# Kernel tuning notes

Hardware: AMD Instinct MI355X
Metric: run time of the kernel (lower is better)

Reference implementation:

```python
import jax, jax.numpy as jnp
import numpy as np

T, B, I, H, C, O = 4096, 8, 256, 512, 1024, 512
SCHEDULE = 1.0
UPPER_T = 0.3
NIND = int((1.0 - SCHEDULE) * (C - 2) * UPPER_T) + 1  # = 1 (argmax WTA)


def setup_inputs() -> dict:
    key = jax.random.key(0)
    ks = jax.random.split(key, 8)
    def lin(k, fan_out, fan_in):
        s = 1.0 / np.sqrt(fan_in)
        kw, kb = jax.random.split(k)
        return (jax.random.uniform(kw, (fan_out, fan_in), jnp.float32, -s, s),
                jax.random.uniform(kb, (fan_out,), jnp.float32, -s, s))
    i2m_w, i2m_b = lin(ks[0], H, I)
    m2h_w, m2h_b = lin(ks[1], C, H)
    h2o_w, h2o_b = lin(ks[2], O, C)
    return {
        "x": jax.random.normal(ks[3], (T, B, I), jnp.float32),
        "hidden1": jnp.zeros((1,), jnp.float32),  # unused dummy (overwritten in torch forward)
        "i2m_w": i2m_w, "i2m_b": i2m_b,
        "m2h_w": m2h_w, "m2h_b": m2h_b,
        "h2o_w": h2o_w, "h2o_b": h2o_b,
    }


def reference(x, hidden1, i2m_w, i2m_b, m2h_w, m2h_b, h2o_w, h2o_b):
    # linear -> relu
    h = jax.nn.relu(jnp.einsum('tbi,hi->tbh', x, i2m_w) + i2m_b)
    # linear -> relu -> concept pre-activations [T,B,C]
    c = jax.nn.relu(jnp.einsum('tbh,ch->tbc', h, m2h_w) + m2h_b)
    # winner-take-all: top-Nind scatter mask (replaces CPU argsort round-trip)
    _, idx = jax.lax.top_k(c, NIND)  # [T,B,NIND]
    t_ix = jnp.arange(c.shape[0])[:, None, None]
    b_ix = jnp.arange(c.shape[1])[None, :, None]
    mask = jnp.zeros_like(c).at[t_ix, b_ix, idx].set(1.0)
    m = c * mask
    # L2 normalize over concept axis
    m = m / jnp.linalg.norm(m, axis=-1, keepdims=True)
    out = jnp.einsum('tbc,oc->tbo', m, h2o_w) + h2o_b
    return jax.nn.log_softmax(out, axis=-1)
```

## Files before the change

kernel.cpp:

```cpp
#include <hip/hip_runtime.h>
#include <stdint.h>

#define M_ROWS 32768
#define I_DIM 256
#define H_DIM 512
#define C_DIM 1024
#define O_DIM 512

typedef __attribute__((ext_vector_type(8))) short bf16x8;
typedef __attribute__((ext_vector_type(4))) float f32x4;

__device__ __forceinline__ ushort bf16_rne(float f) {
    unsigned u = __float_as_uint(f);
    unsigned r = u + 0x7FFFu + ((u >> 16) & 1u);
    return (ushort)(r >> 16);
}
__device__ __forceinline__ float bf16_f32(ushort h) {
    return __uint_as_float(((unsigned)h) << 16);
}
__device__ __forceinline__ void split2(float f, ushort& hi, ushort& mid) {
    hi = bf16_rne(f);
    mid = bf16_rne(f - bf16_f32(hi));
}

__device__ __forceinline__ void async_ld16(const void* g, void* l) {
    __builtin_amdgcn_global_load_lds(
        (const __attribute__((address_space(1))) void*)g,
        (__attribute__((address_space(3))) void*)l, 16, 0, 0);
}

__device__ __forceinline__ unsigned long long packvi(float v, int col) {
    unsigned u = __float_as_uint(v);
    u = (u & 0x80000000u) ? ~u : (u | 0x80000000u);
    return ((unsigned long long)u << 32) | (unsigned)(~col);
}

__global__ __launch_bounds__(256)
void wsplit(const float* __restrict__ W, ushort* __restrict__ hi,
            ushort* __restrict__ mid) {
    int i = (blockIdx.x * 256 + threadIdx.x) * 4;
    float4 v = *(const float4*)(W + i);
    ushort4 hv, mv;
    split2(v.x, hv.x, mv.x);
    split2(v.y, hv.y, mv.y);
    split2(v.z, hv.z, mv.z);
    split2(v.w, hv.w, mv.w);
    *(ushort4*)(hi + i) = hv;
    *(ushort4*)(mid + i) = mv;
}

__global__ __launch_bounds__(256, 3)
void gemm1_mfma(const float* __restrict__ X, const ushort* __restrict__ W1h,
                const ushort* __restrict__ W1m, const float* __restrict__ b1,
                unsigned int* __restrict__ Hp) {
    __shared__ __align__(16) ushort As[2][128 * 32];
    __shared__ __align__(16) ushort Bs[2][128 * 32];
    const int tid = threadIdx.x;
    const int lane = tid & 63, wave = tid >> 6;
    const int wm = wave >> 1, wn = wave & 1;
    const int lcol = lane & 15, quad = lane >> 4;
    const int mBase = blockIdx.x * 128;
    const int nBase = blockIdx.y * 128;
    const int s_row = tid >> 1, s_half = tid & 1;
    const int bplane = wave >> 1;
    const ushort* wp = bplane ? W1m : W1h;
    const int brow0 = (wave & 1) * 64;

    f32x4 acc[4][4];
    #pragma unroll
    for (int i = 0; i < 4; ++i)
        #pragma unroll
        for (int j = 0; j < 4; ++j)
            acc[i][j] = (f32x4){0.f, 0.f, 0.f, 0.f};

    int aoff[4], boff[4];
    #pragma unroll
    for (int t = 0; t < 4; ++t) {
        aoff[t] = (wm * 64 + t * 16 + lcol) * 32 + quad * 8;
        boff[t] = (wn * 64 + t * 16 + lcol) * 32 + quad * 8;
    }

    for (int ks = 0; ks < I_DIM / 32; ++ks) {
        const int k0 = ks * 32;
        const float* ap = X + (size_t)(mBase + s_row) * I_DIM + k0 + s_half * 16;
        float4 f0 = ((const float4*)ap)[0];
        float4 f1 = ((const float4*)ap)[1];
        float4 f2 = ((const float4*)ap)[2];
        float4 f3 = ((const float4*)ap)[3];

        __syncthreads();

        #pragma unroll
        for (int i = 0; i < 4; ++i) {
            int r = brow0 + i * 16;
            const ushort* g = wp + (size_t)(nBase + r + (lane >> 2)) * I_DIM
                              + k0 + (lane & 3) * 8;
            async_ld16(g, &Bs[bplane][r * 32]);
        }

        float f[16];
        *(float4*)&f[0] = f0; *(float4*)&f[4] = f1;
        *(float4*)&f[8] = f2; *(float4*)&f[12] = f3;
        bf16x8 h0, h1, m0, m1;
        #pragma unroll
        for (int j = 0; j < 8; ++j) {
            ushort hu, mu;
            split2(f[j], hu, mu);
            h0[j] = (short)hu; m0[j] = (short)mu;
            split2(f[j + 8], hu, mu);
            h1[j] = (short)hu; m1[j] = (short)mu;
        }
        int dst = s_row * 32 + s_half * 16;
        int sw = (s_row >> 1) & 1;
        *(bf16x8*)&As[0][dst + sw * 8]     = sw ? h1 : h0;
        *(bf16x8*)&As[0][dst + 8 - sw * 8] = sw ? h0 : h1;
        *(bf16x8*)&As[1][dst + sw * 8]     = sw ? m1 : m0;
        *(bf16x8*)&As[1][dst + 8 - sw * 8] = sw ? m0 : m1;

        __syncthreads();

        bf16x8 af[4][2];
        #pragma unroll
        for (int mt = 0; mt < 4; ++mt) {
            af[mt][0] = *(const bf16x8*)&As[0][aoff[mt]];
            af[mt][1] = *(const bf16x8*)&As[1][aoff[mt]];
        }
        #pragma unroll
        for (int nt = 0; nt < 4; ++nt) {
            bf16x8 bh = *(const bf16x8*)&Bs[0][boff[nt]];
            bf16x8 bm = *(const bf16x8*)&Bs[1][boff[nt]];
            #pragma unroll
            for (int mt = 0; mt < 4; ++mt) {
                f32x4 a = acc[mt][nt];
                a = __builtin_amdgcn_mfma_f32_16x16x32_bf16(af[mt][1], bm, a, 0, 0, 0);
                a = __builtin_amdgcn_mfma_f32_16x16x32_bf16(af[mt][1], bh, a, 0, 0, 0);
                a = __builtin_amdgcn_mfma_f32_16x16x32_bf16(af[mt][0], bm, a, 0, 0, 0);
                a = __builtin_amdgcn_mfma_f32_16x16x32_bf16(af[mt][0], bh, a, 0, 0, 0);
                acc[mt][nt] = a;
            }
        }
    }

    #pragma unroll
    for (int nt = 0; nt < 4; ++nt) {
        int col = nBase + wn * 64 + nt * 16 + lcol;
        float bias = b1[col];
        #pragma unroll
        for (int mt = 0; mt < 4; ++mt) {
            #pragma unroll
            for (int r = 0; r < 4; ++r) {
                int row = mBase + wm * 64 + mt * 16 + quad * 4 + r;
                float v = fmaxf(acc[mt][nt][r] + bias, 0.f);
                ushort hu, mu;
                split2(v, hu, mu);
                Hp[(size_t)row * H_DIM + col] = ((unsigned)hu << 16) | (unsigned)mu;
            }
        }
    }
}

__global__ __launch_bounds__(256, 3)
void gemm2_mfma(const unsigned int* __restrict__ Hp,
                const ushort* __restrict__ W2h, const ushort* __restrict__ W2m,
                const float* __restrict__ b2,
                unsigned long long* __restrict__ part) {
    __shared__ __align__(16) ushort As[2][128 * 32];
    __shared__ __align__(16) ushort Bs[2][128 * 32];
    const int tid = threadIdx.x;
    const int lane = tid & 63, wave = tid >> 6;
    const int wm = wave >> 1, wn = wave & 1;
    const int lcol = lane & 15, quad = lane >> 4;
    const int mBase = blockIdx.x * 128;
    const int nBase = blockIdx.y * 128;
    const int s_row = tid >> 1, s_half = tid & 1;
    const int bplane = wave >> 1;
    const ushort* wp = bplane ? W2m : W2h;
    const int brow0 = (wave & 1) * 64;

    f32x4 acc[4][4];
    #pragma unroll
    for (int i = 0; i < 4; ++i)
        #pragma unroll
        for (int j = 0; j < 4; ++j)
            acc[i][j] = (f32x4){0.f, 0.f, 0.f, 0.f};

    int aoff[4], boff[4];
    #pragma unroll
    for (int t = 0; t < 4; ++t) {
        aoff[t] = (wm * 64 + t * 16 + lcol) * 32 + quad * 8;
        boff[t] = (wn * 64 + t * 16 + lcol) * 32 + quad * 8;
    }

    for (int ks = 0; ks < H_DIM / 32; ++ks) {
        const int k0 = ks * 32;
        const unsigned int* ap = Hp + (size_t)(mBase + s_row) * H_DIM + k0 + s_half * 16;
        uint4 a0 = ((const uint4*)ap)[0];
        uint4 a1 = ((const uint4*)ap)[1];
        uint4 a2 = ((const uint4*)ap)[2];
        uint4 a3 = ((const uint4*)ap)[3];

        __syncthreads();

        #pragma unroll
        for (int i = 0; i < 4; ++i) {
            int r = brow0 + i * 16;
            const ushort* g = wp + (size_t)(nBase + r + (lane >> 2)) * H_DIM
                              + k0 + (lane & 3) * 8;
            async_ld16(g, &Bs[bplane][r * 32]);
        }

        unsigned int w[16];
        *(uint4*)&w[0] = a0;  *(uint4*)&w[4] = a1;
        *(uint4*)&w[8] = a2;  *(uint4*)&w[12] = a3;
        bf16x8 h0, h1, m0, m1;
        #pragma unroll
        for (int j = 0; j < 8; ++j) {
            h0[j] = (short)(w[j] >> 16);     m0[j] = (short)(w[j] & 0xFFFFu);
            h1[j] = (short)(w[j + 8] >> 16); m1[j] = (short)(w[j + 8] & 0xFFFFu);
        }
        int dst = s_row * 32 + s_half * 16;
        int sw = (s_row >> 1) & 1;
        *(bf16x8*)&As[0][dst + sw * 8]     = sw ? h1 : h0;
        *(bf16x8*)&As[0][dst + 8 - sw * 8] = sw ? h0 : h1;
        *(bf16x8*)&As[1][dst + sw * 8]     = sw ? m1 : m0;
        *(bf16x8*)&As[1][dst + 8 - sw * 8] = sw ? m0 : m1;

        __syncthreads();

        bf16x8 af[4][2];
        #pragma unroll
        for (int mt = 0; mt < 4; ++mt) {
            af[mt][0] = *(const bf16x8*)&As[0][aoff[mt]];
            af[mt][1] = *(const bf16x8*)&As[1][aoff[mt]];
        }
        #pragma unroll
        for (int nt = 0; nt < 4; ++nt) {
            bf16x8 bh = *(const bf16x8*)&Bs[0][boff[nt]];
            bf16x8 bm = *(const bf16x8*)&Bs[1][boff[nt]];
            #pragma unroll
            for (int mt = 0; mt < 4; ++mt) {
                f32x4 a = acc[mt][nt];
                a = __builtin_amdgcn_mfma_f32_16x16x32_bf16(af[mt][1], bm, a, 0, 0, 0);
                a = __builtin_amdgcn_mfma_f32_16x16x32_bf16(af[mt][1], bh, a, 0, 0, 0);
                a = __builtin_amdgcn_mfma_f32_16x16x32_bf16(af[mt][0], bm, a, 0, 0, 0);
                a = __builtin_amdgcn_mfma_f32_16x16x32_bf16(af[mt][0], bh, a, 0, 0, 0);
                acc[mt][nt] = a;
            }
        }
    }

    unsigned long long best[4][4];
    #pragma unroll
    for (int mt = 0; mt < 4; ++mt)
        #pragma unroll
        for (int r = 0; r < 4; ++r)
            best[mt][r] = 0ull;

    #pragma unroll
    for (int nt = 0; nt < 4; ++nt) {
        int col = nBase + wn * 64 + nt * 16 + lcol;
        float bias = b2[col];
        #pragma unroll
        for (int mt = 0; mt < 4; ++mt) {
            #pragma unroll
            for (int r = 0; r < 4; ++r) {
                float v = acc[mt][nt][r] + bias;
                unsigned long long p = packvi(v, col);
                if (p > best[mt][r]) best[mt][r] = p;
            }
        }
    }
    #pragma unroll
    for (int mt = 0; mt < 4; ++mt)
        #pragma unroll
        for (int r = 0; r < 4; ++r) {
            unsigned long long b = best[mt][r];
            #pragma unroll
            for (int off = 1; off < 16; off <<= 1) {
                unsigned long long o = __shfl_xor((long long)b, off, 64);
                if (o > b) b = o;
            }
            best[mt][r] = b;
        }

    __syncthreads();
    unsigned long long* red = (unsigned long long*)&As[0][0];
    if (lcol == 0) {
        #pragma unroll
        for (int mt = 0; mt < 4; ++mt)
            #pragma unroll
            for (int r = 0; r < 4; ++r)
                red[(wm * 64 + mt * 16 + quad * 4 + r) * 2 + wn] = best[mt][r];
    }
    __syncthreads();
    if (tid < 128) {
        unsigned long long a = red[tid * 2], b = red[tid * 2 + 1];
        part[(size_t)(mBase + tid) * 8 + blockIdx.y] = (a > b) ? a : b;
    }
}

__global__ __launch_bounds__(256)
void argmax_reduce(const unsigned long long* __restrict__ part, int* __restrict__ jstar) {
    int m = blockIdx.x * blockDim.x + threadIdx.x;
    if (m >= M_ROWS) return;
    const unsigned long long* p = part + (size_t)m * 8;
    unsigned long long best = p[0];
    #pragma unroll
    for (int t = 1; t < 8; ++t) {
        unsigned long long q = p[t];
        if (q > best) best = q;
    }
    unsigned u = (unsigned)(best >> 32);
    float v = (u & 0x80000000u) ? __uint_as_float(u ^ 0x80000000u)
                                : __uint_as_float(~u);
    int col = (int)(~(unsigned)best) & (C_DIM - 1);
    jstar[m] = (v > 0.f) ? col : 0;
}

__global__ __launch_bounds__(256)
void ls_table(const float* __restrict__ Wo, const float* __restrict__ bo,
              float* __restrict__ LS) {
    const int j = blockIdx.x;
    const int t = threadIdx.x;
    __shared__ float sred[4];

    float l0 = Wo[(size_t)t * C_DIM + j] + bo[t];
    float l1 = Wo[(size_t)(t + 256) * C_DIM + j] + bo[t + 256];

    float mx = fmaxf(l0, l1);
    #pragma unroll
    for (int off = 1; off < 64; off <<= 1)
        mx = fmaxf(mx, __shfl_xor(mx, off, 64));
    if ((t & 63) == 0) sred[t >> 6] = mx;
    __syncthreads();
    mx = fmaxf(fmaxf(sred[0], sred[1]), fmaxf(sred[2], sred[3]));
    __syncthreads();

    float s = expf(l0 - mx) + expf(l1 - mx);
    #pragma unroll
    for (int off = 1; off < 64; off <<= 1)
        s += __shfl_xor(s, off, 64);
    if ((t & 63) == 0) sred[t >> 6] = s;
    __syncthreads();
    s = sred[0] + sred[1] + sred[2] + sred[3];

    float lse = mx + logf(s);
    LS[(size_t)j * O_DIM + t] = l0 - lse;
    LS[(size_t)j * O_DIM + t + 256] = l1 - lse;
}

__global__ __launch_bounds__(256)
void gather_out(const int* __restrict__ jstar, const float* __restrict__ LS,
                float* __restrict__ out) {
    int idx = blockIdx.x * blockDim.x + threadIdx.x;
    int m = idx >> 7;
    int q = idx & 127;
    float4 v = ((const float4*)LS)[((size_t)jstar[m] << 7) + q];
    ((float4*)out)[idx] = v;
}

extern "C" void kernel_launch(void* const* d_in, const int* in_sizes, int n_in,
                              void* d_out, int out_size, void* d_ws, size_t ws_size,
                              hipStream_t stream) {
    const float* x     = (const float*)d_in[0];
    const float* i2m_w = (const float*)d_in[2];
    const float* i2m_b = (const float*)d_in[3];
    const float* m2h_w = (const float*)d_in[4];
    const float* m2h_b = (const float*)d_in[5];
    const float* h2o_w = (const float*)d_in[6];
    const float* h2o_b = (const float*)d_in[7];
    float* out = (float*)d_out;

    char* ws = (char*)d_ws;
    ushort* w1h = (ushort*)(ws);
    ushort* w1m = (ushort*)(ws + 262144);
    ushort* w2h = (ushort*)(ws + 524288);
    ushort* w2m = (ushort*)(ws + 1572864);
    unsigned long long* part = (unsigned long long*)(ws + 2621440);
    int*   jstar = (int*)(ws + 4718592);
    float* LS    = (float*)(ws);

    unsigned int* Hp = (unsigned int*)d_out;

    wsplit<<<(H_DIM * I_DIM) / 1024, 256, 0, stream>>>(i2m_w, w1h, w1m);
    wsplit<<<(C_DIM * H_DIM) / 1024, 256, 0, stream>>>(m2h_w, w2h, w2m);
    gemm1_mfma<<<dim3(M_ROWS / 128, H_DIM / 128), 256, 0, stream>>>(
        x, w1h, w1m, i2m_b, Hp);
    gemm2_mfma<<<dim3(M_ROWS / 128, C_DIM / 128), 256, 0, stream>>>(
        Hp, w2h, w2m, m2h_b, part);
    argmax_reduce<<<M_ROWS / 256, 256, 0, stream>>>(part, jstar);
    ls_table<<<C_DIM, 256, 0, stream>>>(h2o_w, h2o_b, LS);
    gather_out<<<(M_ROWS * (O_DIM / 4)) / 256, 256, 0, stream>>>(jstar, LS, out);
}
```

Before: 280.9 us.

## Fuse prep kernels, drop mid*mid MFMA, split H planes, atomicMax argmax

The two weight-split kernels, the log-softmax table and the zeroing of the argmax buffer are merged into one prep launch. gemm1 now writes separate hi and mid bf16 planes of H, so gemm2 can fill shared memory directly with async global-to-LDS loads instead of unpacking through registers. The mid*mid MFMA term is dropped in both GEMMs, and occupancy is raised to 4 blocks per SM. The per-row argmax now goes through atomicMax on a single 64-bit slot, which removes the separate reduce kernel. Dropping the mid*mid product lowers precision slightly, and the async LDS path loses the old bank-swizzle on the A tile.

```diff
diff --git a/kernel.cpp b/kernel.cpp
--- a/kernel.cpp
+++ b/kernel.cpp
@@ -36,23 +36,60 @@
 }
 
 __global__ __launch_bounds__(256)
-void wsplit(const float* __restrict__ W, ushort* __restrict__ hi,
-            ushort* __restrict__ mid) {
-    int i = (blockIdx.x * 256 + threadIdx.x) * 4;
-    float4 v = *(const float4*)(W + i);
-    ushort4 hv, mv;
-    split2(v.x, hv.x, mv.x);
-    split2(v.y, hv.y, mv.y);
-    split2(v.z, hv.z, mv.z);
-    split2(v.w, hv.w, mv.w);
-    *(ushort4*)(hi + i) = hv;
-    *(ushort4*)(mid + i) = mv;
-}
-
-__global__ __launch_bounds__(256, 3)
+void prep(const float* __restrict__ W1, ushort* __restrict__ w1h, ushort* __restrict__ w1m,
+          const float* __restrict__ W2, ushort* __restrict__ w2h, ushort* __restrict__ w2m,
+          const float* __restrict__ Wo, const float* __restrict__ bo,
+          float* __restrict__ LS, unsigned long long* __restrict__ part) {
+    __shared__ float sred[4];
+    const int b = blockIdx.x;
+    const int t = threadIdx.x;
+    if (b < 640) {
+        const float* W = (b < 128) ? W1 : W2;
+        ushort* hh = (b < 128) ? w1h : w2h;
+        ushort* mm = (b < 128) ? w1m : w2m;
+        int i = ((b < 128 ? b : b - 128) * 256 + t) * 4;
+        float4 v = *(const float4*)(W + i);
+        ushort4 hv, mv;
+        split2(v.x, hv.x, mv.x);
+        split2(v.y, hv.y, mv.y);
+        split2(v.z, hv.z, mv.z);
+        split2(v.w, hv.w, mv.w);
+        *(ushort4*)(hh + i) = hv;
+        *(ushort4*)(mm + i) = mv;
+    } else if (b < 1664) {
+        const int j = b - 640;
+        float l0 = Wo[(size_t)t * C_DIM + j] + bo[t];
+        float l1 = Wo[(size_t)(t + 256) * C_DIM + j] + bo[t + 256];
+
+        float mx = fmaxf(l0, l1);
+        #pragma unroll
+        for (int off = 1; off < 64; off <<= 1)
+            mx = fmaxf(mx, __shfl_xor(mx, off, 64));
+        if ((t & 63) == 0) sred[t >> 6] = mx;
+        __syncthreads();
+        mx = fmaxf(fmaxf(sred[0], sred[1]), fmaxf(sred[2], sred[3]));
+        __syncthreads();
+
+        float s = expf(l0 - mx) + expf(l1 - mx);
+        #pragma unroll
+        for (int off = 1; off < 64; off <<= 1)
+            s += __shfl_xor(s, off, 64);
+        if ((t & 63) == 0) sred[t >> 6] = s;
+        __syncthreads();
+        s = sred[0] + sred[1] + sred[2] + sred[3];
+
+        float lse = mx + logf(s);
+        LS[(size_t)j * O_DIM + t] = l0 - lse;
+        LS[(size_t)j * O_DIM + t + 256] = l1 - lse;
+    } else {
+        part[(b - 1664) * 256 + t] = 0ull;
+    }
+}
+
+__global__ __launch_bounds__(256, 4)
 void gemm1_mfma(const float* __restrict__ X, const ushort* __restrict__ W1h,
                 const ushort* __restrict__ W1m, const float* __restrict__ b1,
-                unsigned int* __restrict__ Hp) {
+                ushort* __restrict__ Hh, ushort* __restrict__ Hm) {
     __shared__ __align__(16) ushort As[2][128 * 32];
     __shared__ __align__(16) ushort Bs[2][128 * 32];
     const int tid = threadIdx.x;
@@ -65,6 +102,7 @@
     const int bplane = wave >> 1;
     const ushort* wp = bplane ? W1m : W1h;
     const int brow0 = (wave & 1) * 64;
+    const int lrow = lane >> 2, lk = (lane & 3) * 8;
 
     f32x4 acc[4][4];
     #pragma unroll
@@ -93,8 +131,7 @@
         #pragma unroll
         for (int i = 0; i < 4; ++i) {
             int r = brow0 + i * 16;
-            const ushort* g = wp + (size_t)(nBase + r + (lane >> 2)) * I_DIM
-                              + k0 + (lane & 3) * 8;
+            const ushort* g = wp + (size_t)(nBase + r + lrow) * I_DIM + k0 + lk;
             async_ld16(g, &Bs[bplane][r * 32]);
         }
 
@@ -132,7 +169,6 @@
             #pragma unroll
             for (int mt = 0; mt < 4; ++mt) {
                 f32x4 a = acc[mt][nt];
-                a = __builtin_amdgcn_mfma_f32_16x16x32_bf16(af[mt][1], bm, a, 0, 0, 0);
                 a = __builtin_amdgcn_mfma_f32_16x16x32_bf16(af[mt][1], bh, a, 0, 0, 0);
                 a = __builtin_amdgcn_mfma_f32_16x16x32_bf16(af[mt][0], bm, a, 0, 0, 0);
                 a = __builtin_amdgcn_mfma_f32_16x16x32_bf16(af[mt][0], bh, a, 0, 0, 0);
@@ -153,14 +189,15 @@
                 float v = fmaxf(acc[mt][nt][r] + bias, 0.f);
                 ushort hu, mu;
                 split2(v, hu, mu);
-                Hp[(size_t)row * H_DIM + col] = ((unsigned)hu << 16) | (unsigned)mu;
-            }
-        }
-    }
-}
-
-__global__ __launch_bounds__(256, 3)
-void gemm2_mfma(const unsigned int* __restrict__ Hp,
+                Hh[(size_t)row * H_DIM + col] = hu;
+                Hm[(size_t)row * H_DIM + col] = mu;
+            }
+        }
+    }
+}
+
+__global__ __launch_bounds__(256, 4)
+void gemm2_mfma(const ushort* __restrict__ Hh, const ushort* __restrict__ Hm,
                 const ushort* __restrict__ W2h, const ushort* __restrict__ W2m,
                 const float* __restrict__ b2,
                 unsigned long long* __restrict__ part) {
@@ -172,10 +209,16 @@
     const int lcol = lane & 15, quad = lane >> 4;
     const int mBase = blockIdx.x * 128;
     const int nBase = blockIdx.y * 128;
-    const int s_row = tid >> 1, s_half = tid & 1;
-    const int bplane = wave >> 1;
-    const ushort* wp = bplane ? W2m : W2h;
-    const int brow0 = (wave & 1) * 64;
+    const int lrow = lane >> 2, lk = (lane & 3) * 8;
+
+    const ushort* gsrc;
+    ushort* lbase;
+    switch (wave) {
+        case 0: gsrc = Hh  + (size_t)mBase * H_DIM; lbase = As[0]; break;
+        case 1: gsrc = Hm  + (size_t)mBase * H_DIM; lbase = As[1]; break;
+        case 2: gsrc = W2h + (size_t)nBase * H_DIM; lbase = Bs[0]; break;
+        default: gsrc = W2m + (size_t)nBase * H_DIM; lbase = Bs[1]; break;
+    }
 
     f32x4 acc[4][4];
     #pragma unroll
@@ -193,38 +236,12 @@
 
     for (int ks = 0; ks < H_DIM / 32; ++ks) {
         const int k0 = ks * 32;
-        const unsigned int* ap = Hp + (size_t)(mBase + s_row) * H_DIM + k0 + s_half * 16;
-        uint4 a0 = ((const uint4*)ap)[0];
-        uint4 a1 = ((const uint4*)ap)[1];
-        uint4 a2 = ((const uint4*)ap)[2];
-        uint4 a3 = ((const uint4*)ap)[3];
-
-        __syncthreads();
-
-        #pragma unroll
-        for (int i = 0; i < 4; ++i) {
-            int r = brow0 + i * 16;
-            const ushort* g = wp + (size_t)(nBase + r + (lane >> 2)) * H_DIM
-                              + k0 + (lane & 3) * 8;
-            async_ld16(g, &Bs[bplane][r * 32]);
-        }
-
-        unsigned int w[16];
-        *(uint4*)&w[0] = a0;  *(uint4*)&w[4] = a1;
-        *(uint4*)&w[8] = a2;  *(uint4*)&w[12] = a3;
-        bf16x8 h0, h1, m0, m1;
+        __syncthreads();
         #pragma unroll
         for (int j = 0; j < 8; ++j) {
-            h0[j] = (short)(w[j] >> 16);     m0[j] = (short)(w[j] & 0xFFFFu);
-            h1[j] = (short)(w[j + 8] >> 16); m1[j] = (short)(w[j + 8] & 0xFFFFu);
-        }
-        int dst = s_row * 32 + s_half * 16;
-        int sw = (s_row >> 1) & 1;
-        *(bf16x8*)&As[0][dst + sw * 8]     = sw ? h1 : h0;
-        *(bf16x8*)&As[0][dst + 8 - sw * 8] = sw ? h0 : h1;
-        *(bf16x8*)&As[1][dst + sw * 8]     = sw ? m1 : m0;
-        *(bf16x8*)&As[1][dst + 8 - sw * 8] = sw ? m0 : m1;
-
+            const ushort* g = gsrc + (size_t)(j * 16 + lrow) * H_DIM + k0 + lk;
+            async_ld16(g, lbase + j * 512);
+        }
         __syncthreads();
 
         bf16x8 af[4][2];
@@ -240,7 +257,6 @@
             #pragma unroll
             for (int mt = 0; mt < 4; ++mt) {
                 f32x4 a = acc[mt][nt];
-                a = __builtin_amdgcn_mfma_f32_16x16x32_bf16(af[mt][1], bm, a, 0, 0, 0);
                 a = __builtin_amdgcn_mfma_f32_16x16x32_bf16(af[mt][1], bh, a, 0, 0, 0);
                 a = __builtin_amdgcn_mfma_f32_16x16x32_bf16(af[mt][0], bm, a, 0, 0, 0);
                 a = __builtin_amdgcn_mfma_f32_16x16x32_bf16(af[mt][0], bh, a, 0, 0, 0);
@@ -249,114 +265,45 @@
         }
     }
 
-    unsigned long long best[4][4];
-    #pragma unroll
-    for (int mt = 0; mt < 4; ++mt)
-        #pragma unroll
-        for (int r = 0; r < 4; ++r)
-            best[mt][r] = 0ull;
-
-    #pragma unroll
-    for (int nt = 0; nt < 4; ++nt) {
-        int col = nBase + wn * 64 + nt * 16 + lcol;
-        float bias = b2[col];
-        #pragma unroll
-        for (int mt = 0; mt < 4; ++mt) {
-            #pragma unroll
-            for (int r = 0; r < 4; ++r) {
-                float v = acc[mt][nt][r] + bias;
+    #pragma unroll
+    for (int mt = 0; mt < 4; ++mt) {
+        #pragma unroll
+        for (int r = 0; r < 4; ++r) {
+            unsigned long long best = 0ull;
+            #pragma unroll
+            for (int nt = 0; nt < 4; ++nt) {
+                int col = nBase + wn * 64 + nt * 16 + lcol;
+                float v = acc[mt][nt][r] + b2[col];
                 unsigned long long p = packvi(v, col);
-                if (p > best[mt][r]) best[mt][r] = p;
-            }
-        }
-    }
-    #pragma unroll
-    for (int mt = 0; mt < 4; ++mt)
-        #pragma unroll
-        for (int r = 0; r < 4; ++r) {
-            unsigned long long b = best[mt][r];
+                if (p > best) best = p;
+            }
             #pragma unroll
             for (int off = 1; off < 16; off <<= 1) {
-                unsigned long long o = __shfl_xor((long long)b, off, 64);
-                if (o > b) b = o;
-            }
-            best[mt][r] = b;
-        }
-
-    __syncthreads();
-    unsigned long long* red = (unsigned long long*)&As[0][0];
-    if (lcol == 0) {
-        #pragma unroll
-        for (int mt = 0; mt < 4; ++mt)
-            #pragma unroll
-            for (int r = 0; r < 4; ++r)
-                red[(wm * 64 + mt * 16 + quad * 4 + r) * 2 + wn] = best[mt][r];
-    }
-    __syncthreads();
-    if (tid < 128) {
-        unsigned long long a = red[tid * 2], b = red[tid * 2 + 1];
-        part[(size_t)(mBase + tid) * 8 + blockIdx.y] = (a > b) ? a : b;
+                unsigned long long o = __shfl_xor((long long)best, off, 64);
+                if (o > best) best = o;
+            }
+            if (lcol == 0) {
+                int row = mBase + wm * 64 + mt * 16 + quad * 4 + r;
+                atomicMax(&part[row], best);
+            }
+        }
     }
 }
 
 __global__ __launch_bounds__(256)
-void argmax_reduce(const unsigned long long* __restrict__ part, int* __restrict__ jstar) {
-    int m = blockIdx.x * blockDim.x + threadIdx.x;
-    if (m >= M_ROWS) return;
-    const unsigned long long* p = part + (size_t)m * 8;
-    unsigned long long best = p[0];
-    #pragma unroll
-    for (int t = 1; t < 8; ++t) {
-        unsigned long long q = p[t];
-        if (q > best) best = q;
-    }
+void gather_out(const unsigned long long* __restrict__ part,
+                const float* __restrict__ LS, float* __restrict__ out) {
+    const int tid = threadIdx.x;
+    const int row = blockIdx.x * 2 + (tid >> 7);
+    const int q = tid & 127;
+    unsigned long long best = part[row];
     unsigned u = (unsigned)(best >> 32);
     float v = (u & 0x80000000u) ? __uint_as_float(u ^ 0x80000000u)
                                 : __uint_as_float(~u);
     int col = (int)(~(unsigned)best) & (C_DIM - 1);
-    jstar[m] = (v > 0.f) ? col : 0;
-}
-
-__global__ __launch_bounds__(256)
-void ls_table(const float* __restrict__ Wo, const float* __restrict__ bo,
-              float* __restrict__ LS) {
-    const int j = blockIdx.x;
-    const int t = threadIdx.x;
-    __shared__ float sred[4];
-
-    float l0 = Wo[(size_t)t * C_DIM + j] + bo[t];
-    float l1 = Wo[(size_t)(t + 256) * C_DIM + j] + bo[t + 256];
-
-    float mx = fmaxf(l0, l1);
-    #pragma unroll
-    for (int off = 1; off < 64; off <<= 1)
-        mx = fmaxf(mx, __shfl_xor(mx, off, 64));
-    if ((t & 63) == 0) sred[t >> 6] = mx;
-    __syncthreads();
-    mx = fmaxf(fmaxf(sred[0], sred[1]), fmaxf(sred[2], sred[3]));
-    __syncthreads();
-
-    float s = expf(l0 - mx) + expf(l1 - mx);
-    #pragma unroll
-    for (int off = 1; off < 64; off <<= 1)
-        s += __shfl_xor(s, off, 64);
-    if ((t & 63) == 0) sred[t >> 6] = s;
-    __syncthreads();
-    s = sred[0] + sred[1] + sred[2] + sred[3];
-
-    float lse = mx + logf(s);
-    LS[(size_t)j * O_DIM + t] = l0 - lse;
-    LS[(size_t)j * O_DIM + t + 256] = l1 - lse;
-}
-
-__global__ __launch_bounds__(256)
-void gather_out(const int* __restrict__ jstar, const float* __restrict__ LS,
-                float* __restrict__ out) {
-    int idx = blockIdx.x * blockDim.x + threadIdx.x;
-    int m = idx >> 7;
-    int q = idx & 127;
-    float4 v = ((const float4*)LS)[((size_t)jstar[m] << 7) + q];
-    ((float4*)out)[idx] = v;
+    int j = (v > 0.f) ? col : 0;
+    float4 val = ((const float4*)LS)[(size_t)j * 128 + q];
+    ((float4*)out)[(size_t)row * 128 + q] = val;
 }
 
 extern "C" void kernel_launch(void* const* d_in, const int* in_sizes, int n_in,
@@ -376,19 +323,17 @@
     ushort* w1m = (ushort*)(ws + 262144);
     ushort* w2h = (ushort*)(ws + 524288);
     ushort* w2m = (ushort*)(ws + 1572864);
-    unsigned long long* part = (unsigned long long*)(ws + 2621440);
-    int*   jstar = (int*)(ws + 4718592);
-    float* LS    = (float*)(ws);
-
-    unsigned int* Hp = (unsigned int*)d_out;
-
-    wsplit<<<(H_DIM * I_DIM) / 1024, 256, 0, stream>>>(i2m_w, w1h, w1m);
-    wsplit<<<(C_DIM * H_DIM) / 1024, 256, 0, stream>>>(m2h_w, w2h, w2m);
+    float*  LS  = (float*)(ws + 2621440);
+    unsigned long long* part = (unsigned long long*)(ws + 4718592);
+
+    ushort* Hh = (ushort*)d_out;
+    ushort* Hm = Hh + (size_t)M_ROWS * H_DIM;
+
+    prep<<<1792, 256, 0, stream>>>(i2m_w, w1h, w1m, m2h_w, w2h, w2m,
+                                   h2o_w, h2o_b, LS, part);
     gemm1_mfma<<<dim3(M_ROWS / 128, H_DIM / 128), 256, 0, stream>>>(
-        x, w1h, w1m, i2m_b, Hp);
+        x, w1h, w1m, i2m_b, Hh, Hm);
     gemm2_mfma<<<dim3(M_ROWS / 128, C_DIM / 128), 256, 0, stream>>>(
-        Hp, w2h, w2m, m2h_b, part);
-    argmax_reduce<<<M_ROWS / 256, 256, 0, stream>>>(part, jstar);
-    ls_table<<<C_DIM, 256, 0, stream>>>(h2o_w, h2o_b, LS);
-    gather_out<<<(M_ROWS * (O_DIM / 4)) / 256, 256, 0, stream>>>(jstar, LS, out);
-}
+        Hh, Hm, w2h, w2m, m2h_b, part);
+    gather_out<<<M_ROWS / 2, 256, 0, stream>>>(part, LS, out);
+}
```

Result: faster. 260.4 us (-7.3%).
